# Performance work log

Measured on AMD Instinct MI355X. Metric: run time of the kernel, lower is better.

## Reference

```python
import jax, jax.numpy as jnp
import numpy as np

N_MEL = 80
NEG = -1e30  # log-zero sentinel, as in the torch module


def setup_inputs() -> dict:
    key = jax.random.key(0)
    k1, k2, k3, k4 = jax.random.split(key, 4)
    B, txt_T, mel_T = 16, 128, 512
    mu_logvar = jax.random.normal(k1, (B, txt_T, 2 * N_MEL), dtype=jnp.float32)
    melspec = jax.random.normal(k2, (B, N_MEL, mel_T), dtype=jnp.float32)
    text_lengths = jax.random.randint(k3, (B,), txt_T // 2, txt_T + 1, dtype=jnp.int32)
    mel_lengths = jax.random.randint(k4, (B,), mel_T // 2, mel_T + 1, dtype=jnp.int32)
    return dict(mu_logvar=mu_logvar, melspec=melspec,
                text_lengths=text_lengths, mel_lengths=mel_lengths)


def _log_prob_matrix(mu_logvar, melspec):
    # mu_logvar: [B, txt_T, 2*n_mel]; melspec: [B, n_mel, mel_T]
    mu = mu_logvar[:, :, :N_MEL]            # [B, txt_T, n_mel]
    logvar = mu_logvar[:, :, N_MEL:]        # [B, txt_T, n_mel]
    x = jnp.transpose(melspec, (0, 2, 1))   # [B, mel_T, n_mel]
    diff = x[:, None, :, :] - mu[:, :, None, :]          # [B, txt_T, mel_T, n_mel]
    quad = diff * diff * jnp.exp(-logvar)[:, :, None, :] + logvar[:, :, None, :]
    return -0.5 * jnp.mean(quad, axis=3)    # [B, txt_T, mel_T]


def _log_alpha_last(log_prob_matrix, text_lengths, mel_lengths):
    B, txt_T, mel_T = log_prob_matrix.shape
    # init: log_alpha[:, :, 0] = NEG except [:,0,0] = logp[:,0,0]
    init = jnp.full((B, txt_T), NEG, log_prob_matrix.dtype).at[:, 0].set(log_prob_matrix[:, 0, 0])
    logp_t = jnp.moveaxis(log_prob_matrix, 2, 0)  # [mel_T, B, txt_T]

    def step(prev, lp):
        # shift-by-one along text axis (monotonic alignment: stay or advance)
        shifted = jnp.concatenate([jnp.full((B, 1), NEG, prev.dtype), prev[:, :-1]], axis=1)
        cur = jnp.logaddexp(prev + 1e-30, shifted + 1e-30) + lp
        return cur, cur

    _, rest = jax.lax.scan(step, init, logp_t[1:])
    log_alpha = jnp.concatenate([init[None], rest], axis=0)  # [mel_T, B, txt_T]
    b = jnp.arange(B)
    return log_alpha[mel_lengths - 1, b, text_lengths - 1]   # [B]


def reference(mu_logvar, melspec, text_lengths, mel_lengths):
    log_prob_matrix = _log_prob_matrix(mu_logvar, melspec)
    alpha_last = _log_alpha_last(log_prob_matrix, text_lengths, mel_lengths)
    alpha_last = alpha_last / mel_lengths
    mdn_loss = -jnp.mean(alpha_last)
    return (mdn_loss, log_prob_matrix)
```

## Files before the change

### kernel.cpp

```cpp
#include <hip/hip_runtime.h>

#define NEG (-1e30f)
#define LN2F 0.69314718056f

#define B_   16
#define TXT_ 128
#define MEL_ 512
#define NM_  80
#define IT_  8

typedef float vf4 __attribute__((ext_vector_type(4)));

__global__ __launch_bounds__(512) void lp_kernel(
    const float* __restrict__ mu_logvar,
    const float* __restrict__ melspec,
    float* __restrict__ lp_out,
    float* __restrict__ out0)
{
    const int i0 = blockIdx.x * IT_;
    const int b  = blockIdx.y;
    const int t  = threadIdx.x;

    __shared__ float2 s_wb[IT_][NM_];
    __shared__ float  s_cp[IT_ * NM_];
    __shared__ float  s_cc[IT_];

    for (int u = t; u < IT_ * NM_; u += 512) {
        int ii = u / NM_;
        int n  = u - ii * NM_;
        const float* row = mu_logvar + (size_t)(b * TXT_ + i0 + ii) * (2 * NM_);
        float mu = row[n];
        float lv = row[NM_ + n];
        float w  = __expf(-lv);
        s_wb[ii][n] = make_float2(w, -2.f * mu * w);
        s_cp[u]     = mu * mu * w + lv;
    }
    __syncthreads();
    if (t < IT_) {
        float c = 0.f;
        #pragma unroll
        for (int n = 0; n < NM_; ++n) c += s_cp[t * NM_ + n];
        s_cc[t] = c;
    }
    __syncthreads();

    const float* xcol = melspec + (size_t)b * NM_ * MEL_ + t;
    float acc[IT_];
    #pragma unroll
    for (int ii = 0; ii < IT_; ++ii) acc[ii] = 0.f;

    #pragma unroll 4
    for (int n = 0; n < NM_; ++n) {
        float x  = xcol[(size_t)n * MEL_];
        float x2 = x * x;
        #pragma unroll
        for (int ii = 0; ii < IT_; ++ii) {
            float2 wb = s_wb[ii][n];
            acc[ii] = fmaf(wb.x, x2, fmaf(wb.y, x, acc[ii]));
        }
    }

    const size_t rowbase = ((size_t)(b * TXT_ + i0)) * MEL_ + t;
    #pragma unroll
    for (int ii = 0; ii < IT_; ++ii) {
        lp_out[rowbase + (size_t)ii * MEL_] =
            (-0.5f / (float)NM_) * (acc[ii] + s_cc[ii]);
    }

    if (i0 == 0 && b == 0 && t == 0) *out0 = 0.f;
}

__global__ __launch_bounds__(512) void w_kernel(
    const float* __restrict__ lp,
    const int* __restrict__ mel_len,
    float* __restrict__ w)
{
    const int b = blockIdx.x;
    const int t = threadIdx.x;
    const float* src = lp + (size_t)b * TXT_ * MEL_ + t;
    float* dstb = w + (size_t)b * TXT_ * MEL_;

    float m = NEG;
    #pragma unroll 8
    for (int i = 0; i < TXT_; ++i) m = fmaxf(m, src[(size_t)i * MEL_]);

    const float sh = m + LN2F;
    #pragma unroll 8
    for (int i = 0; i < TXT_; ++i)
        dstb[(size_t)i * MEL_ + t] = __expf(src[(size_t)i * MEL_] - sh);

    __shared__ float red[512];
    const int TendM1 = mel_len[b] - 1;
    red[t] = (t >= 1 && t <= TendM1) ? sh : 0.f;
    __syncthreads();
    #pragma unroll
    for (int s = 256; s > 0; s >>= 1) {
        if (t < s) red[t] += red[t + s];
        __syncthreads();
    }
    if (t == 0) {
        float lp00 = lp[(size_t)b * TXT_ * MEL_];
        dstb[(size_t)127 * MEL_] = red[0] + lp00;
    }
}

__device__ __forceinline__ float dpp_shr1_zero(float x) {
    int r = __builtin_amdgcn_update_dpp(
        0, __builtin_bit_cast(int, x), 0x138 , 0xf, 0xf, false);
    return __builtin_bit_cast(float, r);
}

#define DPPMAX(M, CTRL, RM)                                               \
    do {                                                                  \
        int _t = __builtin_amdgcn_update_dpp(                             \
            __builtin_bit_cast(int, M), __builtin_bit_cast(int, M),       \
            CTRL, RM, 0xf, false);                                        \
        M = fmaxf(M, __builtin_bit_cast(float, _t));                      \
    } while (0)

#define GLOAD(DST, PTR) \
    asm volatile("global_load_dwordx4 %0, %1, off" : "=v"(DST) : "v"(PTR))
#define VWAIT(A,B,C,D2) \
    asm volatile("s_waitcnt vmcnt(4)" : "+v"(A), "+v"(B), "+v"(C), "+v"(D2))

__global__ __launch_bounds__(64) void scan_kernel(
    const float* __restrict__ w,
    const int* __restrict__ text_len, const int* __restrict__ mel_len,
    float* __restrict__ out0)
{
    const int b = blockIdx.x;
    const int l = threadIdx.x;
    const float* base = w + (size_t)b * TXT_ * MEL_;
    const int Tend = mel_len[b], TendM1 = Tend - 1;

    const float* row0 = base + (size_t)(2 * l) * MEL_;
    const float* row1 = row0 + MEL_;

    const float musum = base[(size_t)127 * MEL_];

    float s0 = (l == 0) ? 1.f : 0.f;
    float s1 = 0.f;
    float fin0 = 0.f, fin1 = 0.f;
    int   shift_acc = 0, fsh = 0;

    int t_cur = 1;
    int t_pf  = 16;

    vf4 qa0, qa1, qb0, qb1, qc0, qc1, qd0, qd1;
    {
        const float *p0, *p1;
        p0 = row0 + 0;  p1 = row1 + 0;  GLOAD(qa0, p0); GLOAD(qa1, p1);
        p0 = row0 + 4;  p1 = row1 + 4;  GLOAD(qb0, p0); GLOAD(qb1, p1);
        p0 = row0 + 8;  p1 = row1 + 8;  GLOAD(qc0, p0); GLOAD(qc1, p1);
        p0 = row0 + 12; p1 = row1 + 12; GLOAD(qd0, p0); GLOAD(qd1, p1);
    }

    #define STEP(Q0, Q1, COMP)                               \
        do {                                                 \
            float nb  = dpp_shr1_zero(s1);                   \
            float ns0 = (s0 + nb) * (Q0).COMP;               \
            float ns1 = (s1 + s0) * (Q1).COMP;               \
            bool hit = (t_cur == TendM1);                    \
            fin0 = hit ? ns0 : fin0;                         \
            fin1 = hit ? ns1 : fin1;                         \
            fsh  = hit ? shift_acc : fsh;                    \
            s0 = ns0; s1 = ns1; ++t_cur;                     \
        } while (0)

    #define REFILL(Q0, Q1)                                   \
        do {                                                 \
            int tc_ = min(t_pf, MEL_ - 4);                   \
            const float* p0_ = row0 + tc_;                   \
            const float* p1_ = row1 + tc_;                   \
            GLOAD(Q0, p0_); GLOAD(Q1, p1_);                  \
            t_pf += 4;                                       \
        } while (0)

    #define GROUP(QY0,QY1, QX0,QX1)                          \
        do {                                                 \
            VWAIT(QY0, QY1, QX0, QX1);                       \
            STEP(QY0, QY1, y);                               \
            STEP(QY0, QY1, z);                               \
            STEP(QY0, QY1, w);                               \
            REFILL(QY0, QY1);                                \
            STEP(QX0, QX1, x);                               \
        } while (0)

    for (int t0 = 1; t0 <= TendM1; t0 += 16) {
        GROUP(qa0,qa1, qb0,qb1);
        GROUP(qb0,qb1, qc0,qc1);
        GROUP(qc0,qc1, qd0,qd1);
        GROUP(qd0,qd1, qa0,qa1);

        float mm = fmaxf(s0, s1);
        DPPMAX(mm, 0x111, 0xf);
        DPPMAX(mm, 0x112, 0xf);
        DPPMAX(mm, 0x114, 0xf);
        DPPMAX(mm, 0x118, 0xf);
        DPPMAX(mm, 0x142, 0xa);
        DPPMAX(mm, 0x143, 0xc);
        float M = __builtin_bit_cast(
            float, __builtin_amdgcn_readlane(__builtin_bit_cast(int, mm), 63));
        if (M > 0.f) {
            int e;
            (void)frexpf(M, &e);
            float sc = ldexpf(1.f, -e);
            s0 *= sc; s1 *= sc;
            shift_acc += e;
        }
    }
    #undef STEP
    #undef REFILL
    #undef GROUP

    int jstar = text_len[b] - 1;
    float vs = (jstar & 1) ? fin1 : fin0;
    int   vh = (jstar & 1) ? fsh  : fsh;
    vs = __shfl(vs, jstar >> 1);
    vh = __shfl(vh, jstar >> 1);
    if (l == 0) {
        float val = __logf(vs) + (float)vh * LN2F + musum;
        atomicAdd(out0, -(val / (float)Tend) * (1.f / (float)B_));
    }
}

extern "C" void kernel_launch(void* const* d_in, const int* in_sizes, int n_in,
                              void* d_out, int out_size, void* d_ws, size_t ws_size,
                              hipStream_t stream) {
    const float* mu_logvar = (const float*)d_in[0];
    const float* melspec   = (const float*)d_in[1];
    const int*   text_len  = (const int*)d_in[2];
    const int*   mel_len   = (const int*)d_in[3];

    float* out    = (float*)d_out;
    float* lp_out = out + 1;
    float* w_ws   = (float*)d_ws;

    dim3 g1(TXT_ / IT_, B_);
    lp_kernel<<<g1, MEL_, 0, stream>>>(mu_logvar, melspec, lp_out, out);
    w_kernel<<<B_, MEL_, 0, stream>>>(lp_out, mel_len, w_ws);
    scan_kernel<<<B_, 64, 0, stream>>>(w_ws, text_len, mel_len, out);
}
```

Baseline: 125.7 us.

## Transpose exp-weight workspace to time-major and parallelize its kernel across mel tiles

```diff
diff --git a/kernel.cpp b/kernel.cpp
--- a/kernel.cpp
+++ b/kernel.cpp
@@ -1,6 +1,6 @@
 #include <hip/hip_runtime.h>
 
-#define NEG (-1e30f)
+#define NEG  (-1e30f)
 #define LN2F 0.69314718056f
 
 #define B_   16
@@ -9,12 +9,13 @@
 #define NM_  80
 #define IT_  8
 
-typedef float vf4 __attribute__((ext_vector_type(4)));
+typedef float vf2 __attribute__((ext_vector_type(2)));
 
 __global__ __launch_bounds__(512) void lp_kernel(
     const float* __restrict__ mu_logvar,
     const float* __restrict__ melspec,
     float* __restrict__ lp_out,
+    float* __restrict__ wT,
     float* __restrict__ out0)
 {
     const int i0 = blockIdx.x * IT_;
@@ -67,40 +68,64 @@
             (-0.5f / (float)NM_) * (acc[ii] + s_cc[ii]);
     }
 
+    if (i0 == 0 && t == 0) wT[(size_t)b * MEL_ * TXT_] = 0.f;
     if (i0 == 0 && b == 0 && t == 0) *out0 = 0.f;
 }
 
-__global__ __launch_bounds__(512) void w_kernel(
+__global__ __launch_bounds__(256) void wt_kernel(
     const float* __restrict__ lp,
     const int* __restrict__ mel_len,
-    float* __restrict__ w)
+    float* __restrict__ wT)
 {
-    const int b = blockIdx.x;
-    const int t = threadIdx.x;
-    const float* src = lp + (size_t)b * TXT_ * MEL_ + t;
-    float* dstb = w + (size_t)b * TXT_ * MEL_;
-
-    float m = NEG;
-    #pragma unroll 8
-    for (int i = 0; i < TXT_; ++i) m = fmaxf(m, src[(size_t)i * MEL_]);
-
-    const float sh = m + LN2F;
-    #pragma unroll 8
-    for (int i = 0; i < TXT_; ++i)
-        dstb[(size_t)i * MEL_ + t] = __expf(src[(size_t)i * MEL_] - sh);
-
-    __shared__ float red[512];
-    const int TendM1 = mel_len[b] - 1;
-    red[t] = (t >= 1 && t <= TendM1) ? sh : 0.f;
-    __syncthreads();
-    #pragma unroll
-    for (int s = 256; s > 0; s >>= 1) {
-        if (t < s) red[t] += red[t + s];
-        __syncthreads();
-    }
-    if (t == 0) {
-        float lp00 = lp[(size_t)b * TXT_ * MEL_];
-        dstb[(size_t)127 * MEL_] = red[0] + lp00;
+    __shared__ float tileT[32][TXT_ + 1];
+    __shared__ float pmax[32][8];
+    __shared__ float psum[32];
+
+    const int t0  = blockIdx.x * 32;
+    const int b   = blockIdx.y;
+    const int tid = threadIdx.x;
+
+    const float* src = lp + (size_t)b * TXT_ * MEL_ + t0;
+    for (int u = tid; u < TXT_ * 32; u += 256) {
+        int i = u >> 5, c = u & 31;
+        tileT[c][i] = src[(size_t)i * MEL_ + c];
+    }
+    __syncthreads();
+
+    {
+        int tt = tid >> 3, g = tid & 7;
+        float m = NEG;
+        #pragma unroll
+        for (int k = 0; k < 16; ++k) m = fmaxf(m, tileT[tt][g * 16 + k]);
+        pmax[tt][g] = m;
+    }
+    __syncthreads();
+    if (tid < 32) {
+        float m = pmax[tid][0];
+        #pragma unroll
+        for (int g = 1; g < 8; ++g) m = fmaxf(m, pmax[tid][g]);
+        pmax[tid][0] = m;
+        int tg = t0 + tid;
+        int TendM1 = mel_len[b] - 1;
+        psum[tid] = (tg >= 1 && tg <= TendM1) ? (m + LN2F) : 0.f;
+    }
+    __syncthreads();
+
+    float* dstb = wT + (size_t)b * MEL_ * TXT_;
+    for (int u = tid; u < 32 * TXT_; u += 256) {
+        int tt = u >> 7, i = u & 127;
+        int tg = t0 + tt;
+        if (tg != 0)
+            dstb[(size_t)tg * TXT_ + i] =
+                __expf(tileT[tt][i] - pmax[tt][0] - LN2F);
+    }
+
+    if (tid == 0) {
+        float s = 0.f;
+        #pragma unroll
+        for (int k = 0; k < 32; ++k) s += psum[k];
+        if (t0 == 0) s += tileT[0][0];
+        atomicAdd(&dstb[0], s);
     }
 }
 
@@ -118,48 +143,45 @@
         M = fmaxf(M, __builtin_bit_cast(float, _t));                      \
     } while (0)
 
-#define GLOAD(DST, PTR) \
-    asm volatile("global_load_dwordx4 %0, %1, off" : "=v"(DST) : "v"(PTR))
-#define VWAIT(A,B,C,D2) \
-    asm volatile("s_waitcnt vmcnt(4)" : "+v"(A), "+v"(B), "+v"(C), "+v"(D2))
+#define GLOAD2(DST, PTR) \
+    asm volatile("global_load_dwordx2 %0, %1, off" : "=v"(DST) : "v"(PTR))
+#define VWAIT12(A,B,C,D2) \
+    asm volatile("s_waitcnt vmcnt(12)" : "+v"(A), "+v"(B), "+v"(C), "+v"(D2))
 
 __global__ __launch_bounds__(64) void scan_kernel(
-    const float* __restrict__ w,
+    const float* __restrict__ wT,
     const int* __restrict__ text_len, const int* __restrict__ mel_len,
     float* __restrict__ out0)
 {
     const int b = blockIdx.x;
     const int l = threadIdx.x;
-    const float* base = w + (size_t)b * TXT_ * MEL_;
+    const float* base = wT + (size_t)b * MEL_ * TXT_;
+    const float* wb_  = base + 2 * l;
     const int Tend = mel_len[b], TendM1 = Tend - 1;
-
-    const float* row0 = base + (size_t)(2 * l) * MEL_;
-    const float* row1 = row0 + MEL_;
-
-    const float musum = base[(size_t)127 * MEL_];
 
     float s0 = (l == 0) ? 1.f : 0.f;
     float s1 = 0.f;
     float fin0 = 0.f, fin1 = 0.f;
     int   shift_acc = 0, fsh = 0;
-
-    int t_cur = 1;
-    int t_pf  = 16;
-
-    vf4 qa0, qa1, qb0, qb1, qc0, qc1, qd0, qd1;
+    int   t_cur = 1;
+    int   t_pf  = 17;
+
+    vf2 q0,q1,q2,q3,q4,q5,q6,q7,q8,q9,q10,q11,q12,q13,q14,q15;
     {
-        const float *p0, *p1;
-        p0 = row0 + 0;  p1 = row1 + 0;  GLOAD(qa0, p0); GLOAD(qa1, p1);
-        p0 = row0 + 4;  p1 = row1 + 4;  GLOAD(qb0, p0); GLOAD(qb1, p1);
-        p0 = row0 + 8;  p1 = row1 + 8;  GLOAD(qc0, p0); GLOAD(qc1, p1);
-        p0 = row0 + 12; p1 = row1 + 12; GLOAD(qd0, p0); GLOAD(qd1, p1);
-    }
-
-    #define STEP(Q0, Q1, COMP)                               \
+        const float* p;
+        #define INIT(Q, ROW) p = wb_ + (size_t)(ROW) * TXT_; GLOAD2(Q, p)
+        INIT(q0,1);  INIT(q1,2);  INIT(q2,3);   INIT(q3,4);
+        INIT(q4,5);  INIT(q5,6);  INIT(q6,7);   INIT(q7,8);
+        INIT(q8,9);  INIT(q9,10); INIT(q10,11); INIT(q11,12);
+        INIT(q12,13); INIT(q13,14); INIT(q14,15); INIT(q15,16);
+        #undef INIT
+    }
+
+    #define STEP(Q)                                          \
         do {                                                 \
             float nb  = dpp_shr1_zero(s1);                   \
-            float ns0 = (s0 + nb) * (Q0).COMP;               \
-            float ns1 = (s1 + s0) * (Q1).COMP;               \
+            float ns0 = (s0 + nb) * (Q).x;                   \
+            float ns1 = (s1 + s0) * (Q).y;                   \
             bool hit = (t_cur == TendM1);                    \
             fin0 = hit ? ns0 : fin0;                         \
             fin1 = hit ? ns1 : fin1;                         \
@@ -167,30 +189,26 @@
             s0 = ns0; s1 = ns1; ++t_cur;                     \
         } while (0)
 
-    #define REFILL(Q0, Q1)                                   \
+    #define REFILL(Q)                                        \
         do {                                                 \
-            int tc_ = min(t_pf, MEL_ - 4);                   \
-            const float* p0_ = row0 + tc_;                   \
-            const float* p1_ = row1 + tc_;                   \
-            GLOAD(Q0, p0_); GLOAD(Q1, p1_);                  \
-            t_pf += 4;                                       \
+            int rr = min(t_pf, MEL_ - 1);                    \
+            const float* p_ = wb_ + (size_t)rr * TXT_;       \
+            GLOAD2(Q, p_);                                   \
+            ++t_pf;                                          \
         } while (0)
 
-    #define GROUP(QY0,QY1, QX0,QX1)                          \
+    #define GROUP(QA,QB,QC,QD)                               \
         do {                                                 \
-            VWAIT(QY0, QY1, QX0, QX1);                       \
-            STEP(QY0, QY1, y);                               \
-            STEP(QY0, QY1, z);                               \
-            STEP(QY0, QY1, w);                               \
-            REFILL(QY0, QY1);                                \
-            STEP(QX0, QX1, x);                               \
+            VWAIT12(QA,QB,QC,QD);                            \
+            STEP(QA); STEP(QB); STEP(QC); STEP(QD);          \
+            REFILL(QA); REFILL(QB); REFILL(QC); REFILL(QD);  \
         } while (0)
 
     for (int t0 = 1; t0 <= TendM1; t0 += 16) {
-        GROUP(qa0,qa1, qb0,qb1);
-        GROUP(qb0,qb1, qc0,qc1);
-        GROUP(qc0,qc1, qd0,qd1);
-        GROUP(qd0,qd1, qa0,qa1);
+        GROUP(q0,q1,q2,q3);
+        GROUP(q4,q5,q6,q7);
+        GROUP(q8,q9,q10,q11);
+        GROUP(q12,q13,q14,q15);
 
         float mm = fmaxf(s0, s1);
         DPPMAX(mm, 0x111, 0xf);
@@ -215,11 +233,12 @@
 
     int jstar = text_len[b] - 1;
     float vs = (jstar & 1) ? fin1 : fin0;
-    int   vh = (jstar & 1) ? fsh  : fsh;
+    int   vh = fsh;
     vs = __shfl(vs, jstar >> 1);
     vh = __shfl(vh, jstar >> 1);
     if (l == 0) {
-        float val = __logf(vs) + (float)vh * LN2F + musum;
+        float musum = base[0];
+        float val   = __logf(vs) + (float)vh * LN2F + musum;
         atomicAdd(out0, -(val / (float)Tend) * (1.f / (float)B_));
     }
 }
@@ -234,10 +253,11 @@
 
     float* out    = (float*)d_out;
     float* lp_out = out + 1;
-    float* w_ws   = (float*)d_ws;
+    float* wT     = (float*)d_ws;
 
     dim3 g1(TXT_ / IT_, B_);
-    lp_kernel<<<g1, MEL_, 0, stream>>>(mu_logvar, melspec, lp_out, out);
-    w_kernel<<<B_, MEL_, 0, stream>>>(lp_out, mel_len, w_ws);
-    scan_kernel<<<B_, 64, 0, stream>>>(w_ws, text_len, mel_len, out);
-}
+    lp_kernel<<<g1, MEL_, 0, stream>>>(mu_logvar, melspec, lp_out, wT, out);
+    dim3 g2(MEL_ / 32, B_);
+    wt_kernel<<<g2, 256, 0, stream>>>(lp_out, mel_len, wT);
+    scan_kernel<<<B_, 64, 0, stream>>>(wT, text_len, mel_len, out);
+}
```

Result: faster. 102.3 us (-18.6%).
